# Optimization experiments

Hardware: AMD Instinct MI355X
Metric: run time of the kernel (lower is better)

Reference implementation:

```python
import jax, jax.numpy as jnp
import numpy as np


def setup_inputs() -> dict:
    key = jax.random.key(0)
    ks = jax.random.split(key, 6)
    b, l, d, n = 4, 2048, 1024, 16
    scale_d = 1.0 / np.sqrt(d)
    x = jax.random.normal(ks[0], (b, l, d), dtype=jnp.float32)
    W1 = jax.random.normal(ks[1], (d, d), dtype=jnp.float32) * scale_d
    b1 = jnp.zeros((d,), dtype=jnp.float32)
    W2 = jax.random.normal(ks[2], (n, d), dtype=jnp.float32) * scale_d
    b2 = jnp.zeros((n,), dtype=jnp.float32)
    W3 = jax.random.normal(ks[3], (n, d), dtype=jnp.float32) * scale_d
    b3 = jnp.zeros((n,), dtype=jnp.float32)
    A = jax.random.normal(ks[4], (d, n), dtype=jnp.float32) * np.sqrt(2.0 / (d + n))
    return {"x": x, "W1": W1, "b1": b1, "W2": W2, "b2": b2, "W3": W3, "b3": b3, "A": A}


def reference(x, W1, b1, W2, b2, W3, b3, A):
    # delta = softplus(fc1(x)); B = fc2(x); C = fc3(x)
    delta = jax.nn.softplus(jnp.einsum('bld,ed->ble', x, W1) + b1)   # (b,l,d)
    B = jnp.einsum('bld,nd->bln', x, W2) + b2                         # (b,l,n)
    C = jnp.einsum('bld,nd->bln', x, W3) + b3                         # (b,l,n)
    # Discretization: dB = delta \otimes B; dA = exp(delta \otimes A).
    # In the original forward, h is zero-initialized so dA * h == 0 exactly
    # (for both values and gradients); h_new = x[...,None] * dB.
    dB = jnp.einsum('bld,bln->bldn', delta, B)                        # (b,l,d,n)
    h = x[..., None] * dB                                             # (b,l,d,n)
    y = jnp.einsum('bln,bldn->bld', C, h)                             # (b,l,d)
    return y
```

## Files before the change

kernel.cpp:

```cpp
#include <hip/hip_runtime.h>
#include <hip/hip_bf16.h>

typedef __attribute__((ext_vector_type(8))) short bf16x8;
typedef __attribute__((ext_vector_type(8))) unsigned short u16x8;
typedef __attribute__((ext_vector_type(4))) float f32x4;

#define DDIM 1024
#define BM 128
#define BN 128
#define BK 64

__device__ __forceinline__ void gload_lds16(const void* g, void* l) {
  __builtin_amdgcn_global_load_lds((const __attribute__((address_space(1))) void*)g,
                                   (__attribute__((address_space(3))) void*)l,
                                   16, 0, 0);
}

__device__ __forceinline__ unsigned short f2bf(float f) {
  unsigned int u = __float_as_uint(f);
  unsigned int r = (u + 0x7FFFu + ((u >> 16) & 1u)) >> 16;
  return (unsigned short)r;
}

__global__ __launch_bounds__(256) void s6_convert(
    const float* __restrict__ X, const float* __restrict__ W1,
    const float* __restrict__ W2, const float* __restrict__ W3,
    unsigned short* __restrict__ Xbf, unsigned short* __restrict__ W1bf,
    unsigned short* __restrict__ W2bf, unsigned short* __restrict__ W3bf)
{
  const int wid = threadIdx.x >> 6, lane = threadIdx.x & 63;
  const int row = blockIdx.x * 4 + wid;
  const float* src;
  unsigned short* dst;
  if (row < 8192)      { src = X  + (size_t)row * DDIM;        dst = Xbf  + (size_t)row * DDIM; }
  else if (row < 9216) { int r = row - 8192; src = W1 + (size_t)r * DDIM; dst = W1bf + (size_t)r * DDIM; }
  else if (row < 9232) { int r = row - 9216; src = W2 + (size_t)r * DDIM; dst = W2bf + (size_t)r * DDIM; }
  else                 { int r = row - 9232; src = W3 + (size_t)r * DDIM; dst = W3bf + (size_t)r * DDIM; }

  const float4* s4 = reinterpret_cast<const float4*>(src + lane * 16);
  unsigned short u[16];
  #pragma unroll
  for (int j = 0; j < 4; ++j) {
    float4 v = s4[j];
    u[j*4+0] = f2bf(v.x); u[j*4+1] = f2bf(v.y);
    u[j*4+2] = f2bf(v.z); u[j*4+3] = f2bf(v.w);
  }
  u16x8* d8 = reinterpret_cast<u16x8*>(dst + lane * 16);
  u16x8 lo, hi;
  #pragma unroll
  for (int j = 0; j < 8; ++j) { lo[j] = u[j]; hi[j] = u[j + 8]; }
  d8[0] = lo; d8[1] = hi;
}

__global__ __launch_bounds__(128) void s6_s_kernel(
    const unsigned short* __restrict__ Xbf,
    const unsigned short* __restrict__ W2bf,
    const float* __restrict__ b2,
    const unsigned short* __restrict__ W3bf,
    const float* __restrict__ b3,
    float* __restrict__ s_out)
{
  const int wid  = threadIdx.x >> 6;
  const int lane = threadIdx.x & 63;
  const int grp  = blockIdx.x * 2 + wid;
  const int r0   = grp * 16;
  const int row  = lane & 15;
  const int koff = (lane >> 4) * 8;

  const f32x4 z4 = {0.f, 0.f, 0.f, 0.f};
  f32x4 accB = z4, accC = z4;

  const unsigned short* xp  = Xbf  + (size_t)(r0 + row) * DDIM + koff;
  const unsigned short* w2p = W2bf + (size_t)row * DDIM + koff;
  const unsigned short* w3p = W3bf + (size_t)row * DDIM + koff;

  #pragma unroll 4
  for (int k = 0; k < DDIM; k += 32) {
    bf16x8 a  = *reinterpret_cast<const bf16x8*>(xp  + k);
    bf16x8 f2 = *reinterpret_cast<const bf16x8*>(w2p + k);
    bf16x8 f3 = *reinterpret_cast<const bf16x8*>(w3p + k);
    accB = __builtin_amdgcn_mfma_f32_16x16x32_bf16(a, f2, accB, 0, 0, 0);
    accC = __builtin_amdgcn_mfma_f32_16x16x32_bf16(a, f3, accC, 0, 0, 0);
  }

  const int col = lane & 15;
  const float bb = b2[col];
  const float cb = b3[col];
  float p[4];
  #pragma unroll
  for (int q = 0; q < 4; ++q) p[q] = (accB[q] + bb) * (accC[q] + cb);
  #pragma unroll
  for (int msk = 1; msk < 16; msk <<= 1) {
    #pragma unroll
    for (int q = 0; q < 4; ++q) p[q] += __shfl_xor(p[q], msk, 64);
  }
  if (col == 0) {
    const int rbase = r0 + (lane >> 4) * 4;
    #pragma unroll
    for (int q = 0; q < 4; ++q) s_out[rbase + q] = p[q];
  }
}

__global__ __launch_bounds__(256) void s6_main_kernel(
    const unsigned short* __restrict__ Xbf,
    const unsigned short* __restrict__ W1bf,
    const float* __restrict__ b1,
    const float* __restrict__ s_in,
    float* __restrict__ Y)
{
  __shared__ __align__(16) unsigned short lds[2 * 2 * 8192];

  const int tid  = threadIdx.x;
  const int wid  = tid >> 6;
  const int lane = tid & 63;
  const int tile = (blockIdx.x & 7) * 64 + (blockIdx.x >> 3);
  const int rb   = tile >> 3;
  const int cb   = tile & 7;
  const int row0 = rb * BM;
  const int col0 = cb * BN;
  const int wr = wid >> 1, wc = wid & 1;

  const f32x4 z4 = {0.f, 0.f, 0.f, 0.f};
  f32x4 acc[4][4];
  #pragma unroll
  for (int i = 0; i < 4; ++i)
    #pragma unroll
    for (int j = 0; j < 4; ++j)
      acc[i][j] = z4;

  const int srow  = wid * 8 + (lane >> 3);
  const int sdch  = (lane & 7) ^ (lane >> 3);
  const unsigned short* gaBase = Xbf  + (size_t)(row0 + srow) * DDIM + sdch * 8;
  const unsigned short* gbBase = W1bf + (size_t)(col0 + srow) * DDIM + sdch * 8;

  const int fr = lane & 15;
  const int swz0 = (((lane >> 4) + 0) ^ (fr & 7)) * 8;
  const int swz1 = (((lane >> 4) + 4) ^ (fr & 7)) * 8;

#define STAGE(buf, ktElem) do {                                                \
    const unsigned short* sa_ = gaBase + (ktElem);                             \
    const unsigned short* sb_ = gbBase + (ktElem);                             \
    unsigned short* la_ = &lds[(buf) * 16384 + wid * 512];                     \
    unsigned short* lb_ = &lds[(buf) * 16384 + 8192 + wid * 512];              \
    _Pragma("unroll")                                                          \
    for (int seg = 0; seg < 4; ++seg) {                                        \
      gload_lds16(sa_ + seg * 32 * DDIM, la_ + seg * 2048);                    \
      gload_lds16(sb_ + seg * 32 * DDIM, lb_ + seg * 2048);                    \
    }                                                                          \
  } while (0)

  STAGE(0, 0);
  __syncthreads();

  for (int t = 0; t < 16; ++t) {
    const int cur = t & 1;
    if (t < 15) STAGE(cur ^ 1, (t + 1) * BK);

    const unsigned short* Al = &lds[cur * 16384];
    const unsigned short* Bl = &lds[cur * 16384 + 8192];

    #pragma unroll
    for (int ks = 0; ks < 2; ++ks) {
      const int swz = ks ? swz1 : swz0;
      bf16x8 af[4], bfr[4];
      #pragma unroll
      for (int m = 0; m < 4; ++m)
        af[m] = *reinterpret_cast<const bf16x8*>(&Al[(wr * 64 + m * 16 + fr) * BK + swz]);
      #pragma unroll
      for (int n = 0; n < 4; ++n)
        bfr[n] = *reinterpret_cast<const bf16x8*>(&Bl[(wc * 64 + n * 16 + fr) * BK + swz]);
      #pragma unroll
      for (int m = 0; m < 4; ++m)
        #pragma unroll
        for (int n = 0; n < 4; ++n)
          acc[m][n] = __builtin_amdgcn_mfma_f32_16x16x32_bf16(af[m], bfr[n], acc[m][n], 0, 0, 0);
    }
    __syncthreads();
  }
#undef STAGE

  const int orow = (lane >> 4) * 4;
  #pragma unroll
  for (int m = 0; m < 4; ++m) {
    #pragma unroll
    for (int q = 0; q < 4; ++q) {
      const int gr = row0 + wr * 64 + m * 16 + orow + q;
      const float sv = s_in[gr];
      const size_t rbase = (size_t)gr * DDIM;
      #pragma unroll
      for (int n = 0; n < 4; ++n) {
        const int gc = col0 + wc * 64 + n * 16 + fr;
        const float z  = acc[m][n][q] + b1[gc];
        const float sp = fmaxf(z, 0.f) + __logf(1.f + __expf(-fabsf(z)));
        const float xv = __bfloat162float(*(const __hip_bfloat16*)&Xbf[rbase + gc]);
        Y[rbase + gc] = xv * sv * sp;
      }
    }
  }
}

extern "C" void kernel_launch(void* const* d_in, const int* in_sizes, int n_in,
                              void* d_out, int out_size, void* d_ws, size_t ws_size,
                              hipStream_t stream) {
  const float* x  = (const float*)d_in[0];
  const float* W1 = (const float*)d_in[1];
  const float* b1 = (const float*)d_in[2];
  const float* W2 = (const float*)d_in[3];
  const float* b2 = (const float*)d_in[4];
  const float* W3 = (const float*)d_in[5];
  const float* b3 = (const float*)d_in[6];

  char* ws = (char*)d_ws;
  unsigned short* Xbf  = (unsigned short*)(ws);
  unsigned short* W1bf = (unsigned short*)(ws + 16777216);
  unsigned short* W2bf = (unsigned short*)(ws + 16777216 + 2097152);
  unsigned short* W3bf = (unsigned short*)(ws + 16777216 + 2097152 + 32768);
  float*          s_ws = (float*)(ws + 16777216 + 2097152 + 65536);

  s6_convert<<<2312, 256, 0, stream>>>(x, W1, W2, W3, Xbf, W1bf, W2bf, W3bf);
  s6_s_kernel<<<256, 128, 0, stream>>>(Xbf, W2bf, b2, W3bf, b3, s_ws);
  s6_main_kernel<<<512, 256, 0, stream>>>(Xbf, W1bf, b1, s_ws, (float*)d_out);
}
```

Baseline: 51.09 us.

## Fuse B·C row-scale GEMM into main GEMM kernel with explicit waitcnt pipelining

Removes the separate s6_s_kernel. Each main-kernel block now also stages W2/W3 K-tiles into LDS and computes the per-row B and C projections with extra MFMAs alongside the W1 GEMM, then exchanges them through LDS to form the B·C dot product in the epilogue. The loop also replaces __syncthreads with explicit vmcnt waits and raw barriers so the next stage's loads can overlap compute. The cost is that B/C are recomputed redundantly by each of the 8 column blocks, plus extra LDS traffic and registers.

```diff
diff --git a/kernel.cpp b/kernel.cpp
--- a/kernel.cpp
+++ b/kernel.cpp
@@ -52,63 +52,22 @@
   d8[0] = lo; d8[1] = hi;
 }
 
-__global__ __launch_bounds__(128) void s6_s_kernel(
-    const unsigned short* __restrict__ Xbf,
-    const unsigned short* __restrict__ W2bf,
-    const float* __restrict__ b2,
-    const unsigned short* __restrict__ W3bf,
-    const float* __restrict__ b3,
-    float* __restrict__ s_out)
-{
-  const int wid  = threadIdx.x >> 6;
-  const int lane = threadIdx.x & 63;
-  const int grp  = blockIdx.x * 2 + wid;
-  const int r0   = grp * 16;
-  const int row  = lane & 15;
-  const int koff = (lane >> 4) * 8;
-
-  const f32x4 z4 = {0.f, 0.f, 0.f, 0.f};
-  f32x4 accB = z4, accC = z4;
-
-  const unsigned short* xp  = Xbf  + (size_t)(r0 + row) * DDIM + koff;
-  const unsigned short* w2p = W2bf + (size_t)row * DDIM + koff;
-  const unsigned short* w3p = W3bf + (size_t)row * DDIM + koff;
-
-  #pragma unroll 4
-  for (int k = 0; k < DDIM; k += 32) {
-    bf16x8 a  = *reinterpret_cast<const bf16x8*>(xp  + k);
-    bf16x8 f2 = *reinterpret_cast<const bf16x8*>(w2p + k);
-    bf16x8 f3 = *reinterpret_cast<const bf16x8*>(w3p + k);
-    accB = __builtin_amdgcn_mfma_f32_16x16x32_bf16(a, f2, accB, 0, 0, 0);
-    accC = __builtin_amdgcn_mfma_f32_16x16x32_bf16(a, f3, accC, 0, 0, 0);
-  }
-
-  const int col = lane & 15;
-  const float bb = b2[col];
-  const float cb = b3[col];
-  float p[4];
-  #pragma unroll
-  for (int q = 0; q < 4; ++q) p[q] = (accB[q] + bb) * (accC[q] + cb);
-  #pragma unroll
-  for (int msk = 1; msk < 16; msk <<= 1) {
-    #pragma unroll
-    for (int q = 0; q < 4; ++q) p[q] += __shfl_xor(p[q], msk, 64);
-  }
-  if (col == 0) {
-    const int rbase = r0 + (lane >> 4) * 4;
-    #pragma unroll
-    for (int q = 0; q < 4; ++q) s_out[rbase + q] = p[q];
-  }
-}
-
-__global__ __launch_bounds__(256) void s6_main_kernel(
+__global__ __launch_bounds__(256) void s6_main_fused(
     const unsigned short* __restrict__ Xbf,
     const unsigned short* __restrict__ W1bf,
+    const unsigned short* __restrict__ W2bf,
+    const unsigned short* __restrict__ W3bf,
     const float* __restrict__ b1,
-    const float* __restrict__ s_in,
+    const float* __restrict__ b2,
+    const float* __restrict__ b3,
+    unsigned short* __restrict__ XbfDummy,
     float* __restrict__ Y)
 {
-  __shared__ __align__(16) unsigned short lds[2 * 2 * 8192];
+  __shared__ __align__(16) unsigned short lds[2 * 8192 + 2 * 8192 + 2 * 1024 + 2 * 1024];
+  unsigned short* Ab = lds;
+  unsigned short* Bb = lds + 16384;
+  unsigned short* W2b = lds + 32768;
+  unsigned short* W3b = lds + 34816;
 
   const int tid  = threadIdx.x;
   const int wid  = tid >> 6;
@@ -127,11 +86,14 @@
     #pragma unroll
     for (int j = 0; j < 4; ++j)
       acc[i][j] = z4;
+  f32x4 accS[4] = {z4, z4, z4, z4};
 
   const int srow  = wid * 8 + (lane >> 3);
   const int sdch  = (lane & 7) ^ (lane >> 3);
   const unsigned short* gaBase = Xbf  + (size_t)(row0 + srow) * DDIM + sdch * 8;
   const unsigned short* gbBase = W1bf + (size_t)(col0 + srow) * DDIM + sdch * 8;
+  const int wrow = (wid & 1) * 8 + (lane >> 3);
+  const unsigned short* gwBase = (wid < 2 ? W2bf : W3bf) + (size_t)wrow * DDIM + sdch * 8;
 
   const int fr = lane & 15;
   const int swz0 = (((lane >> 4) + 0) ^ (fr & 7)) * 8;
@@ -140,52 +102,90 @@
 #define STAGE(buf, ktElem) do {                                                \
     const unsigned short* sa_ = gaBase + (ktElem);                             \
     const unsigned short* sb_ = gbBase + (ktElem);                             \
-    unsigned short* la_ = &lds[(buf) * 16384 + wid * 512];                     \
-    unsigned short* lb_ = &lds[(buf) * 16384 + 8192 + wid * 512];              \
+    unsigned short* la_ = Ab + (buf) * 8192 + wid * 512;                       \
+    unsigned short* lb_ = Bb + (buf) * 8192 + wid * 512;                       \
     _Pragma("unroll")                                                          \
     for (int seg = 0; seg < 4; ++seg) {                                        \
       gload_lds16(sa_ + seg * 32 * DDIM, la_ + seg * 2048);                    \
       gload_lds16(sb_ + seg * 32 * DDIM, lb_ + seg * 2048);                    \
     }                                                                          \
+    unsigned short* lw_ = (wid < 2 ? W2b : W3b) + (buf) * 1024 + (wid & 1) * 512; \
+    gload_lds16(gwBase + (ktElem), lw_);                                       \
   } while (0)
 
   STAGE(0, 0);
-  __syncthreads();
 
   for (int t = 0; t < 16; ++t) {
     const int cur = t & 1;
-    if (t < 15) STAGE(cur ^ 1, (t + 1) * BK);
-
-    const unsigned short* Al = &lds[cur * 16384];
-    const unsigned short* Bl = &lds[cur * 16384 + 8192];
+    if (t < 15) {
+      STAGE(cur ^ 1, (t + 1) * BK);
+      asm volatile("s_waitcnt vmcnt(9)" ::: "memory");
+    } else {
+      asm volatile("s_waitcnt vmcnt(0)" ::: "memory");
+    }
+    __builtin_amdgcn_s_barrier();
+    __builtin_amdgcn_sched_barrier(0);
+
+    const unsigned short* Al = Ab + cur * 8192;
+    const unsigned short* Bl = Bb + cur * 8192;
+    const unsigned short* Wl = (wc == 0 ? W2b : W3b) + cur * 1024;
 
     #pragma unroll
     for (int ks = 0; ks < 2; ++ks) {
       const int swz = ks ? swz1 : swz0;
-      bf16x8 af[4], bfr[4];
+      bf16x8 af[4], bfr[4], wf;
       #pragma unroll
       for (int m = 0; m < 4; ++m)
         af[m] = *reinterpret_cast<const bf16x8*>(&Al[(wr * 64 + m * 16 + fr) * BK + swz]);
       #pragma unroll
       for (int n = 0; n < 4; ++n)
         bfr[n] = *reinterpret_cast<const bf16x8*>(&Bl[(wc * 64 + n * 16 + fr) * BK + swz]);
-      #pragma unroll
-      for (int m = 0; m < 4; ++m)
+      wf = *reinterpret_cast<const bf16x8*>(&Wl[fr * BK + swz]);
+      #pragma unroll
+      for (int m = 0; m < 4; ++m) {
         #pragma unroll
         for (int n = 0; n < 4; ++n)
           acc[m][n] = __builtin_amdgcn_mfma_f32_16x16x32_bf16(af[m], bfr[n], acc[m][n], 0, 0, 0);
-    }
-    __syncthreads();
+        accS[m] = __builtin_amdgcn_mfma_f32_16x16x32_bf16(af[m], wf, accS[m], 0, 0, 0);
+      }
+    }
+    __builtin_amdgcn_s_barrier();
   }
 #undef STAGE
 
-  const int orow = (lane >> 4) * 4;
+  __syncthreads();
+  float* sEx = (float*)lds;
+  const int n_  = lane & 15;
+  const int rgp = (lane >> 4) * 4;
+  const float bSelf = (wc == 0 ? b2[n_] : b3[n_]);
+  #pragma unroll
+  for (int m = 0; m < 4; ++m)
+    #pragma unroll
+    for (int q = 0; q < 4; ++q)
+      sEx[(wc * 128 + wr * 64 + m * 16 + rgp + q) * 17 + n_] = accS[m][q] + bSelf;
+  __syncthreads();
+
+  float sv[4][4];
   #pragma unroll
   for (int m = 0; m < 4; ++m) {
     #pragma unroll
     for (int q = 0; q < 4; ++q) {
-      const int gr = row0 + wr * 64 + m * 16 + orow + q;
-      const float sv = s_in[gr];
+      const float other = sEx[((wc ^ 1) * 128 + wr * 64 + m * 16 + rgp + q) * 17 + n_];
+      float p = (accS[m][q] + bSelf) * other;
+      p += __shfl_xor(p, 1, 64);
+      p += __shfl_xor(p, 2, 64);
+      p += __shfl_xor(p, 4, 64);
+      p += __shfl_xor(p, 8, 64);
+      sv[m][q] = p;
+    }
+  }
+
+  #pragma unroll
+  for (int m = 0; m < 4; ++m) {
+    #pragma unroll
+    for (int q = 0; q < 4; ++q) {
+      const int gr = row0 + wr * 64 + m * 16 + rgp + q;
+      const float svv = sv[m][q];
       const size_t rbase = (size_t)gr * DDIM;
       #pragma unroll
       for (int n = 0; n < 4; ++n) {
@@ -193,7 +193,7 @@
         const float z  = acc[m][n][q] + b1[gc];
         const float sp = fmaxf(z, 0.f) + __logf(1.f + __expf(-fabsf(z)));
         const float xv = __bfloat162float(*(const __hip_bfloat16*)&Xbf[rbase + gc]);
-        Y[rbase + gc] = xv * sv * sp;
+        Y[rbase + gc] = xv * svv * sp;
       }
     }
   }
@@ -215,9 +215,8 @@
   unsigned short* W1bf = (unsigned short*)(ws + 16777216);
   unsigned short* W2bf = (unsigned short*)(ws + 16777216 + 2097152);
   unsigned short* W3bf = (unsigned short*)(ws + 16777216 + 2097152 + 32768);
-  float*          s_ws = (float*)(ws + 16777216 + 2097152 + 65536);
 
   s6_convert<<<2312, 256, 0, stream>>>(x, W1, W2, W3, Xbf, W1bf, W2bf, W3bf);
-  s6_s_kernel<<<256, 128, 0, stream>>>(Xbf, W2bf, b2, W3bf, b3, s_ws);
-  s6_main_kernel<<<512, 256, 0, stream>>>(Xbf, W1bf, b1, s_ws, (float*)d_out);
-}
+  s6_main_fused<<<512, 256, 0, stream>>>(Xbf, W1bf, W2bf, W3bf, b1, b2, b3,
+                                         nullptr, (float*)d_out);
+}
```

New measurement: 46.43 us. 9.1% less time.
